# Kernel tuning notes

Measured on AMD Instinct MI355X. Metric: run time of the kernel, lower is better.

Reference implementation:

```python
import jax, jax.numpy as jnp
import numpy as np


def setup_inputs() -> dict:
    key = jax.random.key(0)
    kq, kk, kv = jax.random.split(key, 3)
    B, L, H, E = 2, 2048, 16, 64
    queries = jax.random.normal(kq, (B, L, H, E), dtype=jnp.float32)
    keys = jax.random.normal(kk, (B, L, H, E), dtype=jnp.float32)
    values = jax.random.normal(kv, (B, L, H, E), dtype=jnp.float32)
    return {"queries": queries, "keys": keys, "values": values}


def reference(queries, keys, values):
    # queries: [B, L, H, E], keys: [B, S, H, E], values: [B, S, H, D]
    B, L, H, E = queries.shape
    S = keys.shape[1]
    scale = 1.0 / jnp.sqrt(jnp.asarray(E, dtype=queries.dtype))
    # scores: [B, H, L, S]
    scores = jnp.einsum('blhe,bshe->bhls', queries, keys)
    # TriangularCausalMask: mask out strictly-upper-triangular (future) positions
    causal = jnp.triu(jnp.ones((L, S), dtype=bool), k=1)
    neg_inf = jnp.asarray(-jnp.inf, dtype=scores.dtype)
    scores = jnp.where(causal[None, None, :, :], neg_inf, scores)
    A = jax.nn.softmax(scale * scores, axis=-1)  # dropout p=0.0 (eval)
    # V: [B, L, H, D]
    V = jnp.einsum('bhls,bshd->blhd', A, values)
    return V
```

## Files before the change

kernel.cpp:

```cpp
#include <hip/hip_runtime.h>


constexpr int LL = 2048, HH = 16;
constexpr float SL2E = 0.125f * 1.44269504088896340736f;
constexpr float NEG = -1e30f;
constexpr size_t PLANE = 262144;

using bf16x8 = __attribute__((ext_vector_type(8))) short;
using f32x4  = __attribute__((ext_vector_type(4))) float;

__device__ inline float fast_exp2(float x) { return __builtin_amdgcn_exp2f(x); }

__device__ inline unsigned short f2bf(float f) {
    unsigned u = __builtin_bit_cast(unsigned, f);
    return (unsigned short)((u + 0x7fffu + ((u >> 16) & 1u)) >> 16);
}
__device__ inline unsigned pk2r(float lo, float hi) {
    unsigned al = __builtin_bit_cast(unsigned, lo) + 0x8000u;
    unsigned ah = __builtin_bit_cast(unsigned, hi) + 0x8000u;
    return __builtin_amdgcn_perm(ah, al, 0x07060302u);
}
__device__ inline void gload16(const void* g, void* l) {
    __builtin_amdgcn_global_load_lds(
        (const __attribute__((address_space(1))) unsigned int*)g,
        (__attribute__((address_space(3))) unsigned int*)l, 16, 0, 0);
}

__global__ __launch_bounds__(256) void prepack(
    const float* __restrict__ K, const float* __restrict__ V,
    char* __restrict__ wsK, char* __restrict__ wsV)
{
    const int bh = blockIdx.x >> 4;
    const int chunk = blockIdx.x & 15;
    const int b = bh >> 4, h = bh & 15;
    const int s0 = chunk * 128;
    const int tid = threadIdx.x;
    const int wv = tid >> 6, lane = tid & 63;
    const int g = lane >> 4, c16 = lane & 15;

    char* outK = wsK + (size_t)bh * PLANE;
    char* outV = wsV + (size_t)bh * PLANE;

    #pragma unroll
    for (int i = 0; i < 4; ++i) {
        const int idx = i * 256 + tid;
        const int sl = idx >> 3, o = idx & 7;
        const float* src = K + (((size_t)(b * 2048 + s0 + sl)) * 16 + h) * 64 + o * 8;
        float4 f0 = *(const float4*)src;
        float4 f1 = *(const float4*)(src + 4);
        short4 lo = make_short4((short)f2bf(f0.x), (short)f2bf(f0.y),
                                (short)f2bf(f0.z), (short)f2bf(f0.w));
        short4 hi = make_short4((short)f2bf(f1.x), (short)f2bf(f1.y),
                                (short)f2bf(f1.z), (short)f2bf(f1.w));
        char* dst = outK + (s0 + sl) * 128 + ((o << 4) ^ ((sl & 7) << 4));
        *(short4*)dst = lo;
        *(short4*)(dst + 8) = hi;
    }

    const int vrow0 = wv * 4 + g;
    const float* pV = V + (((size_t)(b * 2048 + s0 + vrow0)) * 16 + h) * 64 + c16 * 4;
    const int d = c16 * 4 + g;
    #pragma unroll
    for (int it = 0; it < 8; ++it) {
        float4 vf = *(const float4*)(pV + (size_t)it * 16 * 1024);
        unsigned short a0 = f2bf(vf.x), a1 = f2bf(vf.y),
                       a2 = f2bf(vf.z), a3 = f2bf(vf.w);
        unsigned s1 = (g & 1) ? ((unsigned)a0 | ((unsigned)a2 << 16))
                              : ((unsigned)a1 | ((unsigned)a3 << 16));
        unsigned r1 = __shfl_xor(s1, 16, 64);
        if (g & 1) { a0 = (unsigned short)r1; a2 = (unsigned short)(r1 >> 16); }
        else       { a1 = (unsigned short)r1; a3 = (unsigned short)(r1 >> 16); }
        unsigned s2 = (g & 2) ? ((unsigned)a0 | ((unsigned)a1 << 16))
                              : ((unsigned)a2 | ((unsigned)a3 << 16));
        unsigned r2 = __shfl_xor(s2, 32, 64);
        if (g & 2) { a0 = (unsigned short)r2; a1 = (unsigned short)(r2 >> 16); }
        else       { a2 = (unsigned short)r2; a3 = (unsigned short)(r2 >> 16); }
        const int p_g  = 4 * (it >> 1) + wv;
        const int half = it & 1;
        char* dst = outV + (size_t)d * 4096 + chunk * 256
                  + (((p_g ^ (d & 7)) << 4) + (half << 3));
        *(short4*)dst = make_short4((short)a0, (short)a1, (short)a2, (short)a3);
    }
}

__global__ __launch_bounds__(512, 2) void attn_main(
    const float* __restrict__ Q, const char* __restrict__ wsK,
    const char* __restrict__ wsV, float* __restrict__ Out)
{
    __shared__ __align__(16) short Sh[32768];
    char* ShB = (char*)&Sh[0];

    const int tid  = threadIdx.x;
    const int wv   = tid >> 6;
    const int lane = tid & 63;
    const int g    = lane >> 4;
    const int c16  = lane & 15;
    const int wq   = wv >> 2;
    const int wk   = wv & 3;

    const int i  = blockIdx.x;
    const int bh = ((i & 7) << 2) | ((i >> 3) & 3);
    const int p  = i >> 5;
    const int b = bh >> 4, h = bh & 15;

    const char* planeK = wsK + (size_t)bh * PLANE;
    const char* planeV = wsV + (size_t)bh * PLANE;

    const short ONE = (short)0x3F80;
    const bf16x8 bOnes = {ONE, ONE, ONE, ONE, ONE, ONE, ONE, ONE};

    auto stage = [&](int bi, int t) {
        char* dK = ShB + bi * 16384;
        char* dV = ShB + 32768 + bi * 16384;
        #pragma unroll
        for (int r = 0; r < 2; ++r) {
            const int off = r * 8192 + wv * 1024;
            gload16(planeK + (size_t)t * 16384 + off + lane * 16, dK + off);
        }
        #pragma unroll
        for (int r = 0; r < 2; ++r) {
            const int off = r * 8192 + wv * 1024;
            const int d = r * 32 + wv * 4 + (lane >> 4);
            gload16(planeV + (size_t)d * 4096 + (size_t)t * 256 + (lane & 15) * 16,
                    dV + off);
        }
    };

    #pragma unroll 1
    for (int phase = 0; phase < 2; ++phase) {
        const int qi = phase == 0 ? (15 - p) : p;
        const int q0 = qi * 128;
        const int ntiles = qi + 1;

        bf16x8 bQ[4][2];
        #pragma unroll
        for (int qg = 0; qg < 4; ++qg) {
            const int qrow = q0 + wq * 64 + qg * 16 + c16;
            const float* qp = Q + ((size_t)(b * LL + qrow) * HH + h) * 64 + g * 8;
            #pragma unroll
            for (int es = 0; es < 2; ++es) {
                float4 f0 = *(const float4*)(qp + es * 32);
                float4 f1 = *(const float4*)(qp + es * 32 + 4);
                bf16x8 a;
                a[0] = f2bf(f0.x * SL2E); a[1] = f2bf(f0.y * SL2E);
                a[2] = f2bf(f0.z * SL2E); a[3] = f2bf(f0.w * SL2E);
                a[4] = f2bf(f1.x * SL2E); a[5] = f2bf(f1.y * SL2E);
                a[6] = f2bf(f1.z * SL2E); a[7] = f2bf(f1.w * SL2E);
                bQ[qg][es] = a;
            }
        }

        f32x4 Oacc[4][4];
        #pragma unroll
        for (int qg = 0; qg < 4; ++qg)
            #pragma unroll
            for (int dt = 0; dt < 4; ++dt) Oacc[qg][dt] = (f32x4){0.f, 0.f, 0.f, 0.f};
        f32x4 Lacc[4];
        #pragma unroll
        for (int qg = 0; qg < 4; ++qg) Lacc[qg] = (f32x4){0.f, 0.f, 0.f, 0.f};

        if (phase) __syncthreads();
        int buf = 0;
        stage(0, 0);
        for (int t = 0; t < ntiles; ++t) {
            __syncthreads();
            if (t + 1 < ntiles) stage(buf ^ 1, t + 1);

            const char* Kbuf = ShB + buf * 16384;
            const char* Vbuf = ShB + 32768 + buf * 16384;

            bf16x8 aK[2][2];
            #pragma unroll
            for (int kt2 = 0; kt2 < 2; ++kt2) {
                const int krow = (2 * wk + kt2) * 16 + c16;
                #pragma unroll
                for (int es = 0; es < 2; ++es) {
                    const int off = krow * 128 + (((es * 64) + g * 16) ^ ((krow & 7) << 4));
                    aK[kt2][es] = *(const bf16x8*)(Kbuf + off);
                }
            }
            bf16x8 bV[4];
            #pragma unroll
            for (int dt = 0; dt < 4; ++dt) {
                const int d = dt * 16 + c16;
                const int voff = d * 256 + ((64 * wk + 16 * g) ^ ((d & 7) << 4));
                bV[dt] = *(const bf16x8*)(Vbuf + voff);
            }

            const bool dia = (t == qi);
            #pragma unroll
            for (int qg = 0; qg < 4; ++qg) {
                f32x4 Sv[2];
                __builtin_amdgcn_s_setprio(1);
                #pragma unroll
                for (int kt2 = 0; kt2 < 2; ++kt2) {
                    f32x4 acc = (f32x4){0.f, 0.f, 0.f, 0.f};
                    acc = __builtin_amdgcn_mfma_f32_16x16x32_bf16(aK[kt2][0], bQ[qg][0], acc, 0, 0, 0);
                    acc = __builtin_amdgcn_mfma_f32_16x16x32_bf16(aK[kt2][1], bQ[qg][1], acc, 0, 0, 0);
                    Sv[kt2] = acc;
                }
                __builtin_amdgcn_s_setprio(0);

                const int thr = wq * 64 + qg * 16 + c16;
                unsigned pb[4];
                #pragma unroll
                for (int kt2 = 0; kt2 < 2; ++kt2) {
                    float x0 = Sv[kt2][0], x1 = Sv[kt2][1];
                    float x2 = Sv[kt2][2], x3 = Sv[kt2][3];
                    if (dia) {
                        const int k0 = (2 * wk + kt2) * 16 + 4 * g;
                        x0 = (k0 + 0 <= thr) ? x0 : NEG;
                        x1 = (k0 + 1 <= thr) ? x1 : NEG;
                        x2 = (k0 + 2 <= thr) ? x2 : NEG;
                        x3 = (k0 + 3 <= thr) ? x3 : NEG;
                    }
                    const float p0 = fast_exp2(x0), p1 = fast_exp2(x1);
                    const float p2 = fast_exp2(x2), p3 = fast_exp2(x3);
                    pb[2 * kt2]     = pk2r(p0, p1);
                    pb[2 * kt2 + 1] = pk2r(p2, p3);
                }

                uint4 u; u.x = pb[0]; u.y = pb[1]; u.z = pb[2]; u.w = pb[3];
                const bf16x8 pa = __builtin_bit_cast(bf16x8, u);
                __builtin_amdgcn_s_setprio(1);
                Lacc[qg] = __builtin_amdgcn_mfma_f32_16x16x32_bf16(pa, bOnes, Lacc[qg], 0, 0, 0);
                #pragma unroll
                for (int dt = 0; dt < 4; ++dt)
                    Oacc[qg][dt] = __builtin_amdgcn_mfma_f32_16x16x32_bf16(pa, bV[dt], Oacc[qg][dt], 0, 0, 0);
                __builtin_amdgcn_s_setprio(0);
            }
            buf ^= 1;
        }

        __syncthreads();
        float* Lr = (float*)ShB;
        if (c16 == 0) {
            #pragma unroll
            for (int qg = 0; qg < 4; ++qg)
                *(f32x4*)&Lr[wv * 64 + qg * 16 + g * 4] = Lacc[qg];
        }
        __syncthreads();
        if (wk == 0) {
            #pragma unroll
            for (int qg = 0; qg < 4; ++qg)
                #pragma unroll
                for (int w2 = 1; w2 < 4; ++w2)
                    Lacc[qg] += *(const f32x4*)&Lr[(wq * 4 + w2) * 64 + qg * 16 + g * 4];
        }
        __syncthreads();
        if (wk >= 2) {
            char* sp = ShB + (wq * 2 + (wk - 2)) * 16384;
            #pragma unroll
            for (int qg = 0; qg < 4; ++qg)
                #pragma unroll
                for (int dt = 0; dt < 4; ++dt)
                    *(f32x4*)(sp + (((qg * 4 + g) * 4 + dt) * 16 + c16) * 16) = Oacc[qg][dt];
        }
        __syncthreads();
        if (wk < 2) {
            const char* sp = ShB + (wq * 2 + wk) * 16384;
            #pragma unroll
            for (int qg = 0; qg < 4; ++qg)
                #pragma unroll
                for (int dt = 0; dt < 4; ++dt)
                    Oacc[qg][dt] += *(const f32x4*)(sp + (((qg * 4 + g) * 4 + dt) * 16 + c16) * 16);
        }
        __syncthreads();
        if (wk == 1) {
            char* sp = ShB + wq * 16384;
            #pragma unroll
            for (int qg = 0; qg < 4; ++qg)
                #pragma unroll
                for (int dt = 0; dt < 4; ++dt)
                    *(f32x4*)(sp + (((qg * 4 + g) * 4 + dt) * 16 + c16) * 16) = Oacc[qg][dt];
        }
        __syncthreads();
        if (wk == 0) {
            const char* sp = ShB + wq * 16384;
            #pragma unroll
            for (int qg = 0; qg < 4; ++qg) {
                #pragma unroll
                for (int dt = 0; dt < 4; ++dt)
                    Oacc[qg][dt] += *(const f32x4*)(sp + (((qg * 4 + g) * 4 + dt) * 16 + c16) * 16);
                #pragma unroll
                for (int r = 0; r < 4; ++r) {
                    const float inv = 1.0f / Lacc[qg][r];
                    const int orow = q0 + wq * 64 + qg * 16 + g * 4 + r;
                    float* op = Out + ((size_t)(b * LL + orow) * HH + h) * 64 + c16;
                    #pragma unroll
                    for (int dt = 0; dt < 4; ++dt)
                        op[dt * 16] = Oacc[qg][dt][r] * inv;
                }
            }
        }
    }
}

extern "C" void kernel_launch(void* const* d_in, const int* in_sizes, int n_in,
                              void* d_out, int out_size, void* d_ws, size_t ws_size,
                              hipStream_t stream) {
    const float* Q = (const float*)d_in[0];
    const float* K = (const float*)d_in[1];
    const float* V = (const float*)d_in[2];
    float* out = (float*)d_out;
    (void)in_sizes; (void)n_in; (void)out_size; (void)ws_size;

    char* wsK = (char*)d_ws;
    char* wsV = (char*)d_ws + 32 * PLANE;
    prepack<<<512, 256, 0, stream>>>(K, V, wsK, wsV);
    attn_main<<<256, 512, 0, stream>>>(Q, wsK, wsV, out);
}
```

Before: 49.91 us.

## Use 64-key tiles with 4-deep async pipeline and per-warp causal tile skipping

Restructures the attention main loop so each block processes 64-key tiles with a 4-buffer ring and 3-deep prefetch, using explicit vmcnt waits instead of full syncthreads. The warp layout changes from 2x4 to 4x2 (query x key), so each warp owns 32 query rows. Warps skip key tiles that lie entirely above their causal diagonal. The cross-warp output reduction shrinks to a single LDS exchange. The aim is to cut barrier stalls and wasted masked MFMA work near the diagonal, at the cost of more loop iterations, more per-tile barriers and hand-tuned waitcnt logic.

Result: slower. 51.44 us (+3.1%).

```diff
diff --git a/kernel.cpp b/kernel.cpp
--- a/kernel.cpp
+++ b/kernel.cpp
@@ -95,8 +95,8 @@
     const int lane = tid & 63;
     const int g    = lane >> 4;
     const int c16  = lane & 15;
-    const int wq   = wv >> 2;
-    const int wk   = wv & 3;
+    const int wq   = wv >> 1;
+    const int wk   = wv & 1;
 
     const int i  = blockIdx.x;
     const int bh = ((i & 7) << 2) | ((i >> 3) & 3);
@@ -109,33 +109,27 @@
     const short ONE = (short)0x3F80;
     const bf16x8 bOnes = {ONE, ONE, ONE, ONE, ONE, ONE, ONE, ONE};
 
-    auto stage = [&](int bi, int t) {
-        char* dK = ShB + bi * 16384;
-        char* dV = ShB + 32768 + bi * 16384;
-        #pragma unroll
-        for (int r = 0; r < 2; ++r) {
-            const int off = r * 8192 + wv * 1024;
-            gload16(planeK + (size_t)t * 16384 + off + lane * 16, dK + off);
-        }
-        #pragma unroll
-        for (int r = 0; r < 2; ++r) {
-            const int off = r * 8192 + wv * 1024;
-            const int d = r * 32 + wv * 4 + (lane >> 4);
-            gload16(planeV + (size_t)d * 4096 + (size_t)t * 256 + (lane & 15) * 16,
-                    dV + off);
-        }
+    auto stage = [&](int t) {
+        const int bi = t & 3;
+        gload16(planeK + (size_t)t * 8192 + wv * 1024 + lane * 16,
+                ShB + bi * 8192 + wv * 1024);
+        const int d = wv * 8 + (lane >> 3);
+        gload16(planeV + (size_t)d * 4096 + (t >> 1) * 256 + (t & 1) * 128
+                       + (lane & 7) * 16,
+                ShB + 32768 + bi * 8192 + wv * 1024);
     };
 
     #pragma unroll 1
     for (int phase = 0; phase < 2; ++phase) {
         const int qi = phase == 0 ? (15 - p) : p;
         const int q0 = qi * 128;
-        const int ntiles = qi + 1;
-
-        bf16x8 bQ[4][2];
+        const int nt = 2 * qi + 2;
+        const int rowbase0 = q0 + 32 * wq;
+
+        bf16x8 bQ[2][2];
         #pragma unroll
-        for (int qg = 0; qg < 4; ++qg) {
-            const int qrow = q0 + wq * 64 + qg * 16 + c16;
+        for (int qg = 0; qg < 2; ++qg) {
+            const int qrow = rowbase0 + qg * 16 + c16;
             const float* qp = Q + ((size_t)(b * LL + qrow) * HH + h) * 64 + g * 8;
             #pragma unroll
             for (int es = 0; es < 2; ++es) {
@@ -150,142 +144,129 @@
             }
         }
 
-        f32x4 Oacc[4][4];
+        f32x4 Oacc[2][4];
         #pragma unroll
-        for (int qg = 0; qg < 4; ++qg)
+        for (int qg = 0; qg < 2; ++qg)
             #pragma unroll
             for (int dt = 0; dt < 4; ++dt) Oacc[qg][dt] = (f32x4){0.f, 0.f, 0.f, 0.f};
-        f32x4 Lacc[4];
-        #pragma unroll
-        for (int qg = 0; qg < 4; ++qg) Lacc[qg] = (f32x4){0.f, 0.f, 0.f, 0.f};
+        f32x4 Lacc[2] = {(f32x4){0.f, 0.f, 0.f, 0.f}, (f32x4){0.f, 0.f, 0.f, 0.f}};
 
         if (phase) __syncthreads();
-        int buf = 0;
-        stage(0, 0);
-        for (int t = 0; t < ntiles; ++t) {
-            __syncthreads();
-            if (t + 1 < ntiles) stage(buf ^ 1, t + 1);
-
-            const char* Kbuf = ShB + buf * 16384;
-            const char* Vbuf = ShB + 32768 + buf * 16384;
-
-            bf16x8 aK[2][2];
-            #pragma unroll
-            for (int kt2 = 0; kt2 < 2; ++kt2) {
-                const int krow = (2 * wk + kt2) * 16 + c16;
-                #pragma unroll
-                for (int es = 0; es < 2; ++es) {
-                    const int off = krow * 128 + (((es * 64) + g * 16) ^ ((krow & 7) << 4));
-                    aK[kt2][es] = *(const bf16x8*)(Kbuf + off);
-                }
-            }
-            bf16x8 bV[4];
-            #pragma unroll
-            for (int dt = 0; dt < 4; ++dt) {
-                const int d = dt * 16 + c16;
-                const int voff = d * 256 + ((64 * wk + 16 * g) ^ ((d & 7) << 4));
-                bV[dt] = *(const bf16x8*)(Vbuf + voff);
-            }
-
-            const bool dia = (t == qi);
-            #pragma unroll
-            for (int qg = 0; qg < 4; ++qg) {
-                f32x4 Sv[2];
-                __builtin_amdgcn_s_setprio(1);
+
+        const int pro = nt < 3 ? nt : 3;
+        for (int tt = 0; tt < pro; ++tt) {
+            stage(tt);
+            __builtin_amdgcn_sched_barrier(0);
+        }
+
+        for (int t = 0; t < nt; ++t) {
+            const int rem = nt - 1 - t;
+            if (rem >= 2)      asm volatile("s_waitcnt vmcnt(4)" ::: "memory");
+            else if (rem == 1) asm volatile("s_waitcnt vmcnt(2)" ::: "memory");
+            else               asm volatile("s_waitcnt vmcnt(0)" ::: "memory");
+            __builtin_amdgcn_s_barrier();
+            if (t + 3 < nt) {
+                stage(t + 3);
+                __builtin_amdgcn_sched_barrier(0);
+            }
+
+            if (64 * t + 32 * wk <= rowbase0 + 31) {
+                const int bi = t & 3;
+                const char* Kbuf = ShB + bi * 8192;
+                const char* Vbuf = ShB + 32768 + bi * 8192;
+
+                bf16x8 aK[2][2];
                 #pragma unroll
                 for (int kt2 = 0; kt2 < 2; ++kt2) {
-                    f32x4 acc = (f32x4){0.f, 0.f, 0.f, 0.f};
-                    acc = __builtin_amdgcn_mfma_f32_16x16x32_bf16(aK[kt2][0], bQ[qg][0], acc, 0, 0, 0);
-                    acc = __builtin_amdgcn_mfma_f32_16x16x32_bf16(aK[kt2][1], bQ[qg][1], acc, 0, 0, 0);
-                    Sv[kt2] = acc;
-                }
-                __builtin_amdgcn_s_setprio(0);
-
-                const int thr = wq * 64 + qg * 16 + c16;
-                unsigned pb[4];
-                #pragma unroll
-                for (int kt2 = 0; kt2 < 2; ++kt2) {
-                    float x0 = Sv[kt2][0], x1 = Sv[kt2][1];
-                    float x2 = Sv[kt2][2], x3 = Sv[kt2][3];
-                    if (dia) {
-                        const int k0 = (2 * wk + kt2) * 16 + 4 * g;
-                        x0 = (k0 + 0 <= thr) ? x0 : NEG;
-                        x1 = (k0 + 1 <= thr) ? x1 : NEG;
-                        x2 = (k0 + 2 <= thr) ? x2 : NEG;
-                        x3 = (k0 + 3 <= thr) ? x3 : NEG;
+                    const int krow = (2 * wk + kt2) * 16 + c16;
+                    #pragma unroll
+                    for (int es = 0; es < 2; ++es) {
+                        const int off = krow * 128 + (((es * 64) + g * 16) ^ ((krow & 7) << 4));
+                        aK[kt2][es] = *(const bf16x8*)(Kbuf + off);
                     }
-                    const float p0 = fast_exp2(x0), p1 = fast_exp2(x1);
-                    const float p2 = fast_exp2(x2), p3 = fast_exp2(x3);
-                    pb[2 * kt2]     = pk2r(p0, p1);
-                    pb[2 * kt2 + 1] = pk2r(p2, p3);
-                }
-
-                uint4 u; u.x = pb[0]; u.y = pb[1]; u.z = pb[2]; u.w = pb[3];
-                const bf16x8 pa = __builtin_bit_cast(bf16x8, u);
-                __builtin_amdgcn_s_setprio(1);
-                Lacc[qg] = __builtin_amdgcn_mfma_f32_16x16x32_bf16(pa, bOnes, Lacc[qg], 0, 0, 0);
-                #pragma unroll
-                for (int dt = 0; dt < 4; ++dt)
-                    Oacc[qg][dt] = __builtin_amdgcn_mfma_f32_16x16x32_bf16(pa, bV[dt], Oacc[qg][dt], 0, 0, 0);
-                __builtin_amdgcn_s_setprio(0);
-            }
-            buf ^= 1;
+                }
+                bf16x8 bV[4];
+                #pragma unroll
+                for (int dt = 0; dt < 4; ++dt) {
+                    const int d = dt * 16 + c16;
+                    const int voff = d * 128 + ((64 * wk + 16 * g) ^ ((d & 7) << 4));
+                    bV[dt] = *(const bf16x8*)(Vbuf + voff);
+                }
+
+                #pragma unroll
+                for (int qg = 0; qg < 2; ++qg) {
+                    const int rowbase = rowbase0 + 16 * qg;
+                    f32x4 Sv[2];
+                    __builtin_amdgcn_s_setprio(1);
+                    #pragma unroll
+                    for (int kt2 = 0; kt2 < 2; ++kt2) {
+                        f32x4 acc = (f32x4){0.f, 0.f, 0.f, 0.f};
+                        acc = __builtin_amdgcn_mfma_f32_16x16x32_bf16(aK[kt2][0], bQ[qg][0], acc, 0, 0, 0);
+                        acc = __builtin_amdgcn_mfma_f32_16x16x32_bf16(aK[kt2][1], bQ[qg][1], acc, 0, 0, 0);
+                        Sv[kt2] = acc;
+                    }
+                    __builtin_amdgcn_s_setprio(0);
+
+                    const bool dia = (64 * t + 32 * wk + 31 > rowbase);
+                    const int thr = rowbase + c16 - 64 * t;
+                    unsigned pb[4];
+                    #pragma unroll
+                    for (int kt2 = 0; kt2 < 2; ++kt2) {
+                        float x0 = Sv[kt2][0], x1 = Sv[kt2][1];
+                        float x2 = Sv[kt2][2], x3 = Sv[kt2][3];
+                        if (dia) {
+                            const int k0 = (2 * wk + kt2) * 16 + 4 * g;
+                            x0 = (k0 + 0 <= thr) ? x0 : NEG;
+                            x1 = (k0 + 1 <= thr) ? x1 : NEG;
+                            x2 = (k0 + 2 <= thr) ? x2 : NEG;
+                            x3 = (k0 + 3 <= thr) ? x3 : NEG;
+                        }
+                        const float p0 = fast_exp2(x0), p1 = fast_exp2(x1);
+                        const float p2 = fast_exp2(x2), p3 = fast_exp2(x3);
+                        pb[2 * kt2]     = pk2r(p0, p1);
+                        pb[2 * kt2 + 1] = pk2r(p2, p3);
+                    }
+
+                    uint4 u; u.x = pb[0]; u.y = pb[1]; u.z = pb[2]; u.w = pb[3];
+                    const bf16x8 pa = __builtin_bit_cast(bf16x8, u);
+                    __builtin_amdgcn_s_setprio(1);
+                    Lacc[qg] = __builtin_amdgcn_mfma_f32_16x16x32_bf16(pa, bOnes, Lacc[qg], 0, 0, 0);
+                    #pragma unroll
+                    for (int dt = 0; dt < 4; ++dt)
+                        Oacc[qg][dt] = __builtin_amdgcn_mfma_f32_16x16x32_bf16(pa, bV[dt], Oacc[qg][dt], 0, 0, 0);
+                    __builtin_amdgcn_s_setprio(0);
+                }
+            }
         }
 
         __syncthreads();
         float* Lr = (float*)ShB;
-        if (c16 == 0) {
-            #pragma unroll
-            for (int qg = 0; qg < 4; ++qg)
-                *(f32x4*)&Lr[wv * 64 + qg * 16 + g * 4] = Lacc[qg];
+        char*  Ob = ShB + 1024;
+        if (wk == 1) {
+            if (c16 == 0) {
+                #pragma unroll
+                for (int qg = 0; qg < 2; ++qg)
+                    *(f32x4*)&Lr[((wq * 2 + qg) * 4 + g) * 4] = Lacc[qg];
+            }
+            #pragma unroll
+            for (int qg = 0; qg < 2; ++qg)
+                #pragma unroll
+                for (int dt = 0; dt < 4; ++dt)
+                    *(f32x4*)(Ob + (((wq * 2 + qg) * 4 + dt) * 64 + g * 16 + c16) * 16)
+                        = Oacc[qg][dt];
         }
         __syncthreads();
         if (wk == 0) {
             #pragma unroll
-            for (int qg = 0; qg < 4; ++qg)
-                #pragma unroll
-                for (int w2 = 1; w2 < 4; ++w2)
-                    Lacc[qg] += *(const f32x4*)&Lr[(wq * 4 + w2) * 64 + qg * 16 + g * 4];
-        }
-        __syncthreads();
-        if (wk >= 2) {
-            char* sp = ShB + (wq * 2 + (wk - 2)) * 16384;
-            #pragma unroll
-            for (int qg = 0; qg < 4; ++qg)
+            for (int qg = 0; qg < 2; ++qg) {
+                Lacc[qg] += *(const f32x4*)&Lr[((wq * 2 + qg) * 4 + g) * 4];
                 #pragma unroll
                 for (int dt = 0; dt < 4; ++dt)
-                    *(f32x4*)(sp + (((qg * 4 + g) * 4 + dt) * 16 + c16) * 16) = Oacc[qg][dt];
-        }
-        __syncthreads();
-        if (wk < 2) {
-            const char* sp = ShB + (wq * 2 + wk) * 16384;
-            #pragma unroll
-            for (int qg = 0; qg < 4; ++qg)
-                #pragma unroll
-                for (int dt = 0; dt < 4; ++dt)
-                    Oacc[qg][dt] += *(const f32x4*)(sp + (((qg * 4 + g) * 4 + dt) * 16 + c16) * 16);
-        }
-        __syncthreads();
-        if (wk == 1) {
-            char* sp = ShB + wq * 16384;
-            #pragma unroll
-            for (int qg = 0; qg < 4; ++qg)
-                #pragma unroll
-                for (int dt = 0; dt < 4; ++dt)
-                    *(f32x4*)(sp + (((qg * 4 + g) * 4 + dt) * 16 + c16) * 16) = Oacc[qg][dt];
-        }
-        __syncthreads();
-        if (wk == 0) {
-            const char* sp = ShB + wq * 16384;
-            #pragma unroll
-            for (int qg = 0; qg < 4; ++qg) {
-                #pragma unroll
-                for (int dt = 0; dt < 4; ++dt)
-                    Oacc[qg][dt] += *(const f32x4*)(sp + (((qg * 4 + g) * 4 + dt) * 16 + c16) * 16);
+                    Oacc[qg][dt] += *(const f32x4*)(Ob + (((wq * 2 + qg) * 4 + dt) * 64 + g * 16 + c16) * 16);
                 #pragma unroll
                 for (int r = 0; r < 4; ++r) {
                     const float inv = 1.0f / Lacc[qg][r];
-                    const int orow = q0 + wq * 64 + qg * 16 + g * 4 + r;
+                    const int orow = rowbase0 + 16 * qg + 4 * g + r;
                     float* op = Out + ((size_t)(b * LL + orow) * HH + h) * 64 + c16;
                     #pragma unroll
                     for (int dt = 0; dt < 4; ++dt)
```
